# Optimization experiments

Measured on AMD Instinct MI355X. Metric: run time of the kernel, lower is better.

## Reference

```python
import jax, jax.numpy as jnp
import numpy as np

B, T, C = 512, 80, 512      # batch, encoder seq len, in_channels
H = 256                     # hidden_size
V = 6625                    # out_channels / num_classes


def setup_inputs() -> dict:
    key = jax.random.key(0)
    ks = jax.random.split(key, 12)
    s = lambda *shape: 1.0 / np.sqrt(shape[-1])
    inputs = jax.random.normal(ks[0], (B, T, C), dtype=jnp.float32)
    targets = jax.random.randint(ks[1], (B, 25), 0, V, dtype=jnp.int64)
    i2h_w = jax.random.normal(ks[2], (H, C), dtype=jnp.float32) * s(H, C)
    h2h_w = jax.random.normal(ks[3], (H, H), dtype=jnp.float32) * s(H, H)
    h2h_b = jax.random.normal(ks[4], (H,), dtype=jnp.float32) * 0.01
    score_w = jax.random.normal(ks[5], (1, H), dtype=jnp.float32) * s(1, H)
    gru_in = C + V
    gru_wih = jax.random.normal(ks[6], (3 * H, gru_in), dtype=jnp.float32) * s(3 * H, gru_in)
    gru_whh = jax.random.normal(ks[7], (3 * H, H), dtype=jnp.float32) * s(3 * H, H)
    gru_bih = jax.random.normal(ks[8], (3 * H,), dtype=jnp.float32) * 0.01
    gru_bhh = jax.random.normal(ks[9], (3 * H,), dtype=jnp.float32) * 0.01
    gen_w = jax.random.normal(ks[10], (V, H), dtype=jnp.float32) * s(V, H)
    gen_b = jax.random.normal(ks[11], (V,), dtype=jnp.float32) * 0.01
    return {"inputs": inputs, "targets": targets, "batch_max_length": 25,
            "i2h_w": i2h_w, "h2h_w": h2h_w, "h2h_b": h2h_b, "score_w": score_w,
            "gru_wih": gru_wih, "gru_whh": gru_whh, "gru_bih": gru_bih,
            "gru_bhh": gru_bhh, "gen_w": gen_w, "gen_b": gen_b}


def reference(inputs, targets, batch_max_length, i2h_w, h2h_w, h2h_b, score_w,
              gru_wih, gru_whh, gru_bih, gru_bhh, gen_w, gen_b):
    # batch_H projection is step-invariant: same math as per-step i2h(batch_H)
    batch_H_proj = jnp.einsum('btc,hc->bth', inputs, i2h_w)  # [B,T,H]
    hidden0 = jnp.zeros((inputs.shape[0], H), dtype=inputs.dtype)

    def step(hidden, tgt_t):
        # Bahdanau attention
        ph = hidden @ h2h_w.T + h2h_b                          # [B,H]
        res = jnp.tanh(batch_H_proj + ph[:, None, :])          # [B,T,H]
        e = jnp.einsum('bth,oh->bt', res, score_w)             # [B,T] (score has out dim 1)
        alpha = jax.nn.softmax(e, axis=1)                      # softmax over T
        context = jnp.einsum('bt,btc->bc', alpha, inputs)      # [B,C]
        onehot = jax.nn.one_hot(tgt_t, V, dtype=inputs.dtype)  # [B,V]
        x = jnp.concatenate([context, onehot], axis=1)         # [B,C+V]
        # PyTorch GRUCell
        gi = x @ gru_wih.T + gru_bih                           # [B,3H]
        gh = hidden @ gru_whh.T + gru_bhh                      # [B,3H]
        i_r, i_z, i_n = jnp.split(gi, 3, axis=1)
        h_r, h_z, h_n = jnp.split(gh, 3, axis=1)
        r = jax.nn.sigmoid(i_r + h_r)
        z = jax.nn.sigmoid(i_z + h_z)
        n = jnp.tanh(i_n + r * h_n)
        new_h = (1.0 - z) * n + z * hidden
        return new_h, new_h

    num_steps = batch_max_length
    _, hiddens = jax.lax.scan(step, hidden0, targets[:, :num_steps].T)  # [S,B,H]
    output = jnp.transpose(hiddens, (1, 0, 2))                          # [B,S,H]
    probs = jnp.einsum('bsh,vh->bsv', output, gen_w) + gen_b            # [B,S,V]
    return probs
```

## Files before the change

### kernel.cpp

```cpp
#include <hip/hip_runtime.h>
#include <hip/hip_bf16.h>
#include <hip/hip_fp16.h>
#include <cstdint>

constexpr int kB = 512;
constexpr int kT = 80;
constexpr int kC = 512;
constexpr int kH = 256;
constexpr int kV = 6625;
constexpr int kGIN = kC + kV;

typedef __attribute__((ext_vector_type(8))) short short8;
typedef __attribute__((ext_vector_type(4))) float floatx4;
typedef _Float16 h2v __attribute__((ext_vector_type(2)));
typedef _Float16 half8 __attribute__((ext_vector_type(8)));

__device__ __forceinline__ float fast_tanh(float x) {
  float e = __expf(2.f * x);
  return 1.f - 2.f / (e + 1.f);
}
__device__ __forceinline__ float fast_sig(float x) {
  return 1.f / (1.f + __expf(-x));
}
__device__ __forceinline__ float2 h2f(unsigned int u) {
  union { unsigned int u; __half2 h; } cvt; cvt.u = u;
  return __half22float2(cvt.h);
}
__device__ __forceinline__ h2v as_h2v(unsigned int u) {
  union { unsigned int u; h2v h; } c; c.u = u; return c.h;
}
__device__ __forceinline__ float fdot2f(unsigned int a, unsigned int b, float c) {
#if __has_builtin(__builtin_amdgcn_fdot2)
  return __builtin_amdgcn_fdot2(as_h2v(a), as_h2v(b), c, false);
#else
  h2v av = as_h2v(a), bv = as_h2v(b);
  return (float)av[0] * (float)bv[0] + (float)av[1] * (float)bv[1] + c;
#endif
}

__device__ __forceinline__ void gld_lds16(const void* g, void* l) {
  __builtin_amdgcn_global_load_lds(
      (const __attribute__((address_space(1))) void*)(uintptr_t)g,
      (__attribute__((address_space(3))) void*)(uintptr_t)l, 16, 0, 0);
}

__global__ __launch_bounds__(256) void cvt_bf16(const float* __restrict__ x,
                                                __hip_bfloat16* __restrict__ y,
                                                int n) {
  int i = blockIdx.x * 256 + threadIdx.x;
  if (i < n) y[i] = __float2bfloat16(x[i]);
}

__global__ __launch_bounds__(256) void cvt_fp16x4(const float* __restrict__ x,
                                                  __half* __restrict__ y) {
  int i = (blockIdx.x * 256 + threadIdx.x) * 4;
  float4 v = *(const float4*)(x + i);
  __half2 h01 = __floats2half2_rn(v.x, v.y);
  __half2 h23 = __floats2half2_rn(v.z, v.w);
  uint2 u;
  u.x = *reinterpret_cast<unsigned int*>(&h01);
  u.y = *reinterpret_cast<unsigned int*>(&h23);
  *(uint2*)(y + i) = u;
}

__global__ __launch_bounds__(256) void cvt_wh(const float* __restrict__ h2h,
                                              const float* __restrict__ whh,
                                              __half* __restrict__ wH) {
  const int n = blockIdx.x, c = threadIdx.x;
  float v = (n < kH) ? h2h[(size_t)n * kH + c] : whh[(size_t)(n - kH) * kH + c];
  wH[(size_t)n * kH + c] = __float2half(v);
}

__global__ __launch_bounds__(256) void cvt_wih(const float* __restrict__ wih,
                                               __half* __restrict__ wihH) {
  const int n = blockIdx.x, t = threadIdx.x;
  wihH[(size_t)n * kC + t] = __float2half(wih[(size_t)n * kGIN + t]);
  wihH[(size_t)n * kC + 256 + t] = __float2half(wih[(size_t)n * kGIN + 256 + t]);
}

__global__ __launch_bounds__(256) void wt_transpose(const float* __restrict__ wih,
                                                    const float* __restrict__ bih,
                                                    float* __restrict__ WT) {
  __shared__ float tile[32][33];
  const int vb = blockIdx.x * 32, nb = blockIdx.y * 32;
  const int tx = threadIdx.x & 31, ty0 = threadIdx.x >> 5;
#pragma unroll
  for (int i = 0; i < 4; ++i) {
    int n = nb + ty0 + i * 8;
    int v = vb + tx;
    tile[ty0 + i * 8][tx] = (v < kV) ? wih[(size_t)n * kGIN + kC + v] : 0.f;
  }
  __syncthreads();
  const float bb = bih[nb + tx];
#pragma unroll
  for (int i = 0; i < 4; ++i) {
    int v = vb + ty0 + i * 8;
    if (v < kV) WT[(size_t)v * 768 + nb + tx] = tile[tx][ty0 + i * 8] + bb;
  }
}

__global__ __launch_bounds__(256) void proj_gemm_f16(
    const __half* __restrict__ A, const __half* __restrict__ W,
    float* __restrict__ C) {
  constexpr int K = kC, ldc = kH;
  __shared__ __align__(16) _Float16 As[128 * 32];
  __shared__ __align__(16) _Float16 Ws[128 * 32];
  const int tid = threadIdx.x;
  const int wave = tid >> 6, lane = tid & 63;
  const int m0 = blockIdx.x * 128, n0 = blockIdx.y * 128;
  floatx4 acc[4][4] = {};
  const int lr = lane & 15;
  const int lkb = (lane >> 4) * 8;
  const int mloc = (wave & 1) * 64;
  const int nloc = (wave >> 1) * 64;
  const int srow = wave * 16 + (lane >> 2);
  const int skq = (lane & 3) * 8;
  for (int kt = 0; kt < K; kt += 32) {
#pragma unroll
    for (int r = 0; r < 2; ++r) {
      int rowA = r * 64 + srow;
      const __half* ga = A + (size_t)(m0 + rowA) * K + kt + skq;
      gld_lds16(ga, (char*)As + (size_t)(r * 64 + wave * 16) * 64);
      const __half* gw = W + (size_t)(n0 + rowA) * K + kt + skq;
      gld_lds16(gw, (char*)Ws + (size_t)(r * 64 + wave * 16) * 64);
    }
    __syncthreads();
    half8 af[4], wf[4];
#pragma unroll
    for (int i = 0; i < 4; ++i)
      af[i] = *(const half8*)(As + (mloc + i * 16 + lr) * 32 + lkb);
#pragma unroll
    for (int j = 0; j < 4; ++j)
      wf[j] = *(const half8*)(Ws + (nloc + j * 16 + lr) * 32 + lkb);
#pragma unroll
    for (int i = 0; i < 4; ++i)
#pragma unroll
      for (int j = 0; j < 4; ++j)
        acc[i][j] = __builtin_amdgcn_mfma_f32_16x16x32_f16(af[i], wf[j], acc[i][j], 0, 0, 0);
    __syncthreads();
  }
#pragma unroll
  for (int i = 0; i < 4; ++i) {
#pragma unroll
    for (int j = 0; j < 4; ++j) {
      int col = n0 + nloc + j * 16 + lr;
      int rowb = m0 + mloc + i * 16 + ((lane >> 4) << 2);
#pragma unroll
      for (int r = 0; r < 4; ++r)
        C[(size_t)(rowb + r) * ldc + col] = acc[i][j][r];
    }
  }
}

__global__ __launch_bounds__(512, 2) void fused_steps(
    const __half* __restrict__ inH,
    const float* __restrict__ proj,
    const int*   __restrict__ targets,
    const __half* __restrict__ wHp,
    const float* __restrict__ h2h_b, const float* __restrict__ bhh,
    const __half* __restrict__ wihHp,
    const float* __restrict__ WT,
    const float* __restrict__ score_w,
    __hip_bfloat16* __restrict__ hidd,
    int S) {
  __shared__ __align__(16) float hid_s[kH];
  __shared__ __align__(16) _Float16 hidh_s[kH];
  __shared__ __align__(16) float phgh_s[1024];
  __shared__ __align__(16) _Float16 ctxh_s[kC];
  __shared__ __align__(16) float cst[kC];
  __shared__ __align__(16) float gi_s[768];
  __shared__ float e_s[kT];
  const int tid = threadIdx.x;
  const int bid = blockIdx.x;
  const int r0 = bid;
  const int wave = tid >> 6, lane = tid & 63;
  const int g = tid >> 3, q = tid & 7;
  const _Float16* wH = (const _Float16*)wHp;
  const _Float16* wihH = (const _Float16*)wihHp;

  if (tid < kH) { hid_s[tid] = 0.f; hidh_s[tid] = (_Float16)0.f; }

  const float4 s4 = *(const float4*)(score_w + lane * 4);

  float4 pr[10];
#pragma unroll
  for (int k = 0; k < 10; ++k) {
    const int t = wave + 8 * k;
    pr[k] = *(const float4*)(proj + ((size_t)r0 * kT + t) * kH + lane * 4);
  }
  __syncthreads();

  const int rot = bid % 12;

  for (int s = 0; s < S; ++s) {
#pragma unroll
    for (int i = 0; i < 4; ++i) {
      const int n = g + (((i + bid) & 3) << 6);
      const _Float16* wr = wH + (size_t)n * kH;
      float a0 = 0.f;
#pragma unroll
      for (int p = 0; p < 4; ++p) {
        const int c = p * 64 + q * 8;
        uint4 wv = *(const uint4*)(wr + c);
        uint4 hv = *(const uint4*)(&hidh_s[c]);
        a0 = fdot2f(wv.x, hv.x, a0);
        a0 = fdot2f(wv.y, hv.y, a0);
        a0 = fdot2f(wv.z, hv.z, a0);
        a0 = fdot2f(wv.w, hv.w, a0);
      }
      a0 += __shfl_xor(a0, 1); a0 += __shfl_xor(a0, 2); a0 += __shfl_xor(a0, 4);
      if (q == 0) phgh_s[n] = a0 + h2h_b[n];
    }
    __syncthreads();

    {
      float4 ph4 = *(const float4*)(&phgh_s[lane * 4]);
#pragma unroll
      for (int k = 0; k < 10; ++k) {
        const int t = wave + 8 * k;
        float part = fast_tanh(pr[k].x + ph4.x) * s4.x +
                     fast_tanh(pr[k].y + ph4.y) * s4.y +
                     fast_tanh(pr[k].z + ph4.z) * s4.z +
                     fast_tanh(pr[k].w + ph4.w) * s4.w;
#pragma unroll
        for (int off = 32; off > 0; off >>= 1) part += __shfl_xor(part, off);
        if (lane == 0) e_s[t] = part;
      }
    }
    __syncthreads();

    if (wave == 0) {
      float v0 = e_s[lane];
      float v1 = (lane < kT - 64) ? e_s[64 + lane] : -1e30f;
      float mx = fmaxf(v0, v1);
#pragma unroll
      for (int off = 32; off > 0; off >>= 1) mx = fmaxf(mx, __shfl_xor(mx, off));
      float x0 = __expf(v0 - mx);
      float x1 = (lane < kT - 64) ? __expf(v1 - mx) : 0.f;
      float sm = x0 + x1;
#pragma unroll
      for (int off = 32; off > 0; off >>= 1) sm += __shfl_xor(sm, off);
      float inv = 1.f / sm;
      e_s[lane] = x0 * inv;
      if (lane < kT - 64) e_s[64 + lane] = x1 * inv;
    }
    __syncthreads();

    {
      const int sub = tid >> 8, c2 = (tid & 255) * 2;
      const __half* ib = inH + (size_t)r0 * kT * kC + c2;
      float a0 = 0.f, a1 = 0.f;
      const int t0 = sub * 40;
#pragma unroll 4
      for (int t = t0; t < t0 + 40; ++t) {
        const float al = e_s[t];
        float2 v = h2f(*(const unsigned int*)(ib + (size_t)t * kC));
        a0 += al * v.x; a1 += al * v.y;
      }
      if (sub) { cst[c2] = a0; cst[c2 + 1] = a1; }
      __syncthreads();
      if (!sub) {
        ctxh_s[c2] = (_Float16)(a0 + cst[c2]);
        ctxh_s[c2 + 1] = (_Float16)(a1 + cst[c2 + 1]);
      }
    }
    __syncthreads();

#pragma unroll 2
    for (int i = 0; i < 12; ++i) {
      int io = i + rot; if (io >= 12) io -= 12;
      const int n = g + (io << 6);
      const _Float16* wr = wihH + (size_t)n * kC;
      float a0 = 0.f, b0 = 0.f;
#pragma unroll
      for (int p = 0; p < 8; p += 2) {
        const int c0 = p * 64 + q * 8;
        const int c1 = c0 + 64;
        uint4 wv0 = *(const uint4*)(wr + c0);
        uint4 wv1 = *(const uint4*)(wr + c1);
        uint4 xv0 = *(const uint4*)(&ctxh_s[c0]);
        uint4 xv1 = *(const uint4*)(&ctxh_s[c1]);
        a0 = fdot2f(wv0.x, xv0.x, a0);
        a0 = fdot2f(wv0.y, xv0.y, a0);
        a0 = fdot2f(wv0.z, xv0.z, a0);
        a0 = fdot2f(wv0.w, xv0.w, a0);
        b0 = fdot2f(wv1.x, xv1.x, b0);
        b0 = fdot2f(wv1.y, xv1.y, b0);
        b0 = fdot2f(wv1.z, xv1.z, b0);
        b0 = fdot2f(wv1.w, xv1.w, b0);
      }
      a0 += b0;
      a0 += __shfl_xor(a0, 1); a0 += __shfl_xor(a0, 2); a0 += __shfl_xor(a0, 4);
      if (q == 0) gi_s[n] = a0;
    }
#pragma unroll 2
    for (int i = 0; i < 12; ++i) {
      int io = i + rot; if (io >= 12) io -= 12;
      const int m = g + (io << 6);
      const _Float16* wr = wH + (size_t)(256 + m) * kH;
      float a0 = 0.f;
#pragma unroll
      for (int p = 0; p < 4; ++p) {
        const int c = p * 64 + q * 8;
        uint4 wv = *(const uint4*)(wr + c);
        uint4 hv = *(const uint4*)(&hidh_s[c]);
        a0 = fdot2f(wv.x, hv.x, a0);
        a0 = fdot2f(wv.y, hv.y, a0);
        a0 = fdot2f(wv.z, hv.z, a0);
        a0 = fdot2f(wv.w, hv.w, a0);
      }
      a0 += __shfl_xor(a0, 1); a0 += __shfl_xor(a0, 2); a0 += __shfl_xor(a0, 4);
      if (q == 0) phgh_s[256 + m] = a0 + bhh[m];
    }
    __syncthreads();

    if (tid < kH) {
      const int h = tid;
      const int tg = targets[(size_t)r0 * S + s];
      const float* wtr = WT + (size_t)tg * 768;
      float i_r = gi_s[h] + wtr[h];
      float i_z = gi_s[kH + h] + wtr[kH + h];
      float i_n = gi_s[2 * kH + h] + wtr[2 * kH + h];
      float h_r = phgh_s[kH + h];
      float h_z = phgh_s[2 * kH + h];
      float h_n = phgh_s[3 * kH + h];
      float hv = hid_s[h];
      float rr = fast_sig(i_r + h_r);
      float z = fast_sig(i_z + h_z);
      float nn = fast_tanh(i_n + rr * h_n);
      float o = (1.f - z) * nn + z * hv;
      hid_s[h] = o;
      hidh_s[h] = (_Float16)o;
      hidd[((size_t)r0 * S + s) * kH + h] = __float2bfloat16(o);
    }
    __syncthreads();
  }
}

__global__ __launch_bounds__(256) void final_gemm(
    const __hip_bfloat16* __restrict__ A, const __hip_bfloat16* __restrict__ W,
    const float* __restrict__ bias, float* __restrict__ C, int M, int N, int K) {
  __shared__ __align__(16) short As[128 * 32];
  __shared__ __align__(16) short Ws[128 * 32];
  const int tid = threadIdx.x;
  const int wave = tid >> 6, lane = tid & 63;
  const int m0 = blockIdx.x * 128, n0 = blockIdx.y * 128;
  floatx4 acc[4][4] = {};
  const int lr = lane & 15;
  const int lkb = (lane >> 4) * 8;
  const int mloc = (wave & 1) * 64;
  const int nloc = (wave >> 1) * 64;
  const int srow = wave * 16 + (lane >> 2);
  const int skq = (lane & 3) * 8;
  for (int kt = 0; kt < K; kt += 32) {
#pragma unroll
    for (int r = 0; r < 2; ++r) {
      int rowA = r * 64 + srow;
      const __hip_bfloat16* ga = A + (size_t)(m0 + rowA) * K + kt + skq;
      gld_lds16(ga, (char*)As + (size_t)(r * 64 + wave * 16) * 64);
      int rowW = n0 + rowA;
      if (rowW > N - 1) rowW = N - 1;
      const __hip_bfloat16* gw = W + (size_t)rowW * K + kt + skq;
      gld_lds16(gw, (char*)Ws + (size_t)(r * 64 + wave * 16) * 64);
    }
    __syncthreads();
    short8 af[4], wf[4];
#pragma unroll
    for (int i = 0; i < 4; ++i)
      af[i] = *(const short8*)(As + (mloc + i * 16 + lr) * 32 + lkb);
#pragma unroll
    for (int j = 0; j < 4; ++j)
      wf[j] = *(const short8*)(Ws + (nloc + j * 16 + lr) * 32 + lkb);
#pragma unroll
    for (int i = 0; i < 4; ++i)
#pragma unroll
      for (int j = 0; j < 4; ++j)
        acc[i][j] = __builtin_amdgcn_mfma_f32_16x16x32_bf16(af[i], wf[j], acc[i][j], 0, 0, 0);
    __syncthreads();
  }
#pragma unroll
  for (int i = 0; i < 4; ++i) {
#pragma unroll
    for (int j = 0; j < 4; ++j) {
      int col = n0 + nloc + j * 16 + lr;
      if (col < N) {
        int rowb = m0 + mloc + i * 16 + ((lane >> 4) << 2);
        float bs = bias[col];
#pragma unroll
        for (int r = 0; r < 4; ++r)
          C[(size_t)(rowb + r) * N + col] = acc[i][j][r] + bs;
      }
    }
  }
}

extern "C" void kernel_launch(void* const* d_in, const int* in_sizes, int n_in,
                              void* d_out, int out_size, void* d_ws, size_t ws_size,
                              hipStream_t stream) {
  const float* inputs  = (const float*)d_in[0];
  const int*   targets = (const int*)d_in[1];
  const float* i2h_w   = (const float*)d_in[3];
  const float* h2h_w   = (const float*)d_in[4];
  const float* h2h_b   = (const float*)d_in[5];
  const float* score_w = (const float*)d_in[6];
  const float* gru_wih = (const float*)d_in[7];
  const float* gru_whh = (const float*)d_in[8];
  const float* gru_bih = (const float*)d_in[9];
  const float* gru_bhh = (const float*)d_in[10];
  const float* gen_w   = (const float*)d_in[11];
  const float* gen_b   = (const float*)d_in[12];
  float* out = (float*)d_out;
  const int S = out_size / (kB * kV);

  char* ws = (char*)d_ws;
  size_t off = 0;
  auto alloc = [&](size_t bytes) {
    void* p = ws + off;
    off += (bytes + 255) & ~(size_t)255;
    return p;
  };
  float* proj = (float*)alloc((size_t)kB * kT * kH * 4);
  float* WT   = (float*)alloc((size_t)kV * 768 * 4);
  __half* inH = (__half*)alloc((size_t)kB * kT * kC * 2);
  __half* wH  = (__half*)alloc((size_t)1024 * kH * 2);
  __half* wihH = (__half*)alloc((size_t)768 * kC * 2);
  __half* i2hH = (__half*)alloc((size_t)kH * kC * 2);
  __hip_bfloat16* hidd = (__hip_bfloat16*)alloc((size_t)kB * S * kH * 2);
  __hip_bfloat16* gw16 = (__hip_bfloat16*)alloc((size_t)kV * kH * 2);

  cvt_bf16<<<dim3((kV * kH + 255) / 256), 256, 0, stream>>>(gen_w, gw16, kV * kH);
  cvt_fp16x4<<<dim3(kB * kT * kC / 4 / 256), 256, 0, stream>>>(inputs, inH);
  cvt_fp16x4<<<dim3(kH * kC / 4 / 256), 256, 0, stream>>>(i2h_w, i2hH);
  cvt_wh<<<dim3(1024), 256, 0, stream>>>(h2h_w, gru_whh, wH);
  cvt_wih<<<dim3(768), 256, 0, stream>>>(gru_wih, wihH);
  wt_transpose<<<dim3((kV + 31) / 32, 768 / 32), 256, 0, stream>>>(gru_wih, gru_bih, WT);

  proj_gemm_f16<<<dim3(kB * kT / 128, kH / 128), 256, 0, stream>>>(inH, i2hH, proj);

  fused_steps<<<dim3(kB), 512, 0, stream>>>(
      inH, proj, targets, wH, h2h_b, gru_bhh, wihH, WT, score_w, hidd, S);

  final_gemm<<<dim3(kB * S / 128, (kV + 127) / 128), 256, 0, stream>>>(
      hidd, gw16, gen_b, out, kB * S, kV, kH);
}
```

Measured before the change: 1.556 ms.

## Store attention projection in fp16 LDS, raise occupancy, remap final GEMM blocks

```diff
diff --git a/kernel.cpp b/kernel.cpp
--- a/kernel.cpp
+++ b/kernel.cpp
@@ -101,7 +101,7 @@
 
 __global__ __launch_bounds__(256) void proj_gemm_f16(
     const __half* __restrict__ A, const __half* __restrict__ W,
-    float* __restrict__ C) {
+    __half* __restrict__ C) {
   constexpr int K = kC, ldc = kH;
   __shared__ __align__(16) _Float16 As[128 * 32];
   __shared__ __align__(16) _Float16 Ws[128 * 32];
@@ -147,14 +147,14 @@
       int rowb = m0 + mloc + i * 16 + ((lane >> 4) << 2);
 #pragma unroll
       for (int r = 0; r < 4; ++r)
-        C[(size_t)(rowb + r) * ldc + col] = acc[i][j][r];
-    }
-  }
-}
-
-__global__ __launch_bounds__(512, 2) void fused_steps(
+        C[(size_t)(rowb + r) * ldc + col] = __float2half(acc[i][j][r]);
+    }
+  }
+}
+
+__global__ __launch_bounds__(512, 4) void fused_steps(
     const __half* __restrict__ inH,
-    const float* __restrict__ proj,
+    const __half* __restrict__ projH,
     const int*   __restrict__ targets,
     const __half* __restrict__ wHp,
     const float* __restrict__ h2h_b, const float* __restrict__ bhh,
@@ -163,6 +163,7 @@
     const float* __restrict__ score_w,
     __hip_bfloat16* __restrict__ hidd,
     int S) {
+  __shared__ __align__(16) _Float16 projh_s[kT * kH];
   __shared__ __align__(16) float hid_s[kH];
   __shared__ __align__(16) _Float16 hidh_s[kH];
   __shared__ __align__(16) float phgh_s[1024];
@@ -182,11 +183,11 @@
 
   const float4 s4 = *(const float4*)(score_w + lane * 4);
 
-  float4 pr[10];
-#pragma unroll
-  for (int k = 0; k < 10; ++k) {
-    const int t = wave + 8 * k;
-    pr[k] = *(const float4*)(proj + ((size_t)r0 * kT + t) * kH + lane * 4);
+  {
+    const uint4* gp = (const uint4*)(projH + (size_t)r0 * kT * kH);
+    uint4* lp = (uint4*)projh_s;
+#pragma unroll
+    for (int k = 0; k < 5; ++k) lp[k * 512 + tid] = gp[k * 512 + tid];
   }
   __syncthreads();
 
@@ -218,10 +219,12 @@
 #pragma unroll
       for (int k = 0; k < 10; ++k) {
         const int t = wave + 8 * k;
-        float part = fast_tanh(pr[k].x + ph4.x) * s4.x +
-                     fast_tanh(pr[k].y + ph4.y) * s4.y +
-                     fast_tanh(pr[k].z + ph4.z) * s4.z +
-                     fast_tanh(pr[k].w + ph4.w) * s4.w;
+        uint2 pv = *(const uint2*)(&projh_s[t * kH + lane * 4]);
+        float2 p01 = h2f(pv.x), p23 = h2f(pv.y);
+        float part = fast_tanh(p01.x + ph4.x) * s4.x +
+                     fast_tanh(p01.y + ph4.y) * s4.y +
+                     fast_tanh(p23.x + ph4.z) * s4.z +
+                     fast_tanh(p23.y + ph4.w) * s4.w;
 #pragma unroll
         for (int off = 32; off > 0; off >>= 1) part += __shfl_xor(part, off);
         if (lane == 0) e_s[t] = part;
@@ -344,7 +347,9 @@
   __shared__ __align__(16) short Ws[128 * 32];
   const int tid = threadIdx.x;
   const int wave = tid >> 6, lane = tid & 63;
-  const int m0 = blockIdx.x * 128, n0 = blockIdx.y * 128;
+  const int u = blockIdx.x;
+  const int idx = (u & 7) * 650 + (u >> 3);
+  const int m0 = (idx % 100) * 128, n0 = (idx / 100) * 128;
   floatx4 acc[4][4] = {};
   const int lr = lane & 15;
   const int lkb = (lane >> 4) * 8;
@@ -419,7 +424,7 @@
     off += (bytes + 255) & ~(size_t)255;
     return p;
   };
-  float* proj = (float*)alloc((size_t)kB * kT * kH * 4);
+  __half* projH = (__half*)alloc((size_t)kB * kT * kH * 2);
   float* WT   = (float*)alloc((size_t)kV * 768 * 4);
   __half* inH = (__half*)alloc((size_t)kB * kT * kC * 2);
   __half* wH  = (__half*)alloc((size_t)1024 * kH * 2);
@@ -435,11 +440,11 @@
   cvt_wih<<<dim3(768), 256, 0, stream>>>(gru_wih, wihH);
   wt_transpose<<<dim3((kV + 31) / 32, 768 / 32), 256, 0, stream>>>(gru_wih, gru_bih, WT);
 
-  proj_gemm_f16<<<dim3(kB * kT / 128, kH / 128), 256, 0, stream>>>(inH, i2hH, proj);
+  proj_gemm_f16<<<dim3(kB * kT / 128, kH / 128), 256, 0, stream>>>(inH, i2hH, projH);
 
   fused_steps<<<dim3(kB), 512, 0, stream>>>(
-      inH, proj, targets, wH, h2h_b, gru_bhh, wihH, WT, score_w, hidd, S);
-
-  final_gemm<<<dim3(kB * S / 128, (kV + 127) / 128), 256, 0, stream>>>(
+      inH, projH, targets, wH, h2h_b, gru_bhh, wihH, WT, score_w, hidd, S);
+
+  final_gemm<<<dim3(100 * 52), 256, 0, stream>>>(
       hidd, gw16, gen_b, out, kB * S, kV, kH);
 }
```

Measured after the change: 1.849 ms. +18.8%, slower.
